# Kernel optimization log

Hardware: AMD Instinct MI355X
Metric: run time of the kernel (lower is better)

Reference implementation:

```python
import math
import jax, jax.numpy as jnp
import numpy as np

N_HEAD = 32
LAYER_NUMBER = 10  # cancels out: beta*alibi*L + alpha*QK^T*L = alibi + QK^T/sqrt(d)


def build_alibi(seq_len, n_head, dtype):
    # Faithful port of BLOOM's build_alibi_tensor -> [n_head, 1, seq_len]
    cp2 = 2 ** math.floor(math.log2(n_head))
    base = 2.0 ** (-(2.0 ** -(math.log2(cp2) - 3)))
    slopes = base ** np.arange(1, 1 + cp2)
    if cp2 != n_head:
        extra_base = 2.0 ** (-(2.0 ** -(math.log2(2 * cp2) - 3)))
        num_rem = min(cp2, n_head - cp2)
        slopes = np.concatenate([slopes, extra_base ** np.arange(1, 1 + 2 * num_rem, 2)])
    alibi = slopes[:, None, None] * np.arange(seq_len)[None, None, :]
    return jnp.asarray(alibi, dtype)


def setup_inputs() -> dict:
    key = jax.random.key(0)
    ks = jax.random.split(key, 6)
    B, S, H = 4, 1024, 4096
    return {
        "hidden_states": jax.random.normal(ks[0], (B, S, H), jnp.float32),
        "residual": jax.random.normal(ks[1], (B, S, H), jnp.float32),
        "qkv_w": jax.random.normal(ks[2], (3 * H, H), jnp.float32) * 0.02,
        "qkv_b": jnp.zeros((3 * H,), jnp.float32),
        "dense_w": jax.random.normal(ks[3], (H, H), jnp.float32) * 0.02,
        "dense_b": jnp.zeros((H,), jnp.float32),
    }


def reference(hidden_states, residual, qkv_w, qkv_b, dense_w, dense_b):
    B, S, H = hidden_states.shape
    nh = N_HEAD
    d = H // nh
    # fused qkv projection: [B,S,3H] -> [B,S,nh,3d] -> split
    mixed = (hidden_states @ qkv_w.T + qkv_b).reshape(B, S, nh, 3 * d)
    q, k, v = jnp.split(mixed, 3, axis=-1)  # each [B,S,nh,d]

    alibi = build_alibi(S, nh, hidden_states.dtype)  # [nh,1,S]
    # beta*alibi + alpha*QK^T, then *layer_number in scaled softmax == alibi + QK^T/sqrt(d)
    scores = jnp.einsum("bqhd,bkhd->bhqk", q, k) / math.sqrt(d) + alibi[None]  # [B,nh,S,S]

    causal = jnp.tril(jnp.ones((S, S), bool))  # [S,S], True = attend
    scores = jnp.where(causal, scores, jnp.asarray(-10000.0, scores.dtype))
    # softmax in fp32 (attention_softmax_in_fp32), then zero masked entries like *(~padded_causal_mask)
    probs = jax.nn.softmax(scores.astype(jnp.float32), axis=-1) * causal
    probs = probs.astype(v.dtype)

    ctx = jnp.einsum("bhqk,bkhd->bqhd", probs, v).reshape(B, S, H)
    out = ctx @ dense_w.T + dense_b + residual  # dropout_add with p=0 / eval
    return out
```

## Files before the change

kernel.cpp:

```cpp
#include <hip/hip_runtime.h>
#include <hip/hip_bf16.h>

typedef __attribute__((ext_vector_type(8))) short bf16x8;
typedef __attribute__((ext_vector_type(4))) short short4v;
typedef __attribute__((ext_vector_type(4))) float f32x4;

#define MFMA16(A, B, C) __builtin_amdgcn_mfma_f32_16x16x32_bf16((A), (B), (C), 0, 0, 0)
#define GLDS16(g, l)                                                            \
  __builtin_amdgcn_global_load_lds(                                             \
      (const __attribute__((address_space(1))) void*)(g),                       \
      (__attribute__((address_space(3))) void*)(l), 16, 0, 0)

__device__ __forceinline__ short f2bf(float f) {
  union { float f; unsigned u; } v; v.f = f;
  return (short)((v.u + 0x7fffu + ((v.u >> 16) & 1u)) >> 16);
}

__device__ __forceinline__ void blk_barrier() {
  asm volatile("" ::: "memory");
  __builtin_amdgcn_s_barrier();
  asm volatile("" ::: "memory");
}

__global__ __launch_bounds__(256) void cvt_kernel(const float* __restrict__ in,
                                                  short* __restrict__ out, int n4) {
  int i = blockIdx.x * 256 + threadIdx.x;
  const int stride = gridDim.x * 256;
  for (; i < n4; i += stride) {
    f32x4 v = ((const f32x4*)in)[i];
    short4v o;
    o[0] = f2bf(v[0]); o[1] = f2bf(v[1]); o[2] = f2bf(v[2]); o[3] = f2bf(v[3]);
    ((short4v*)out)[i] = o;
  }
}

__global__ __launch_bounds__(512, 2) void gemm_bt8(const short* __restrict__ A,
                                                   const short* __restrict__ B,
                                                   const float* __restrict__ bias,
                                                   const float* __restrict__ resid,
                                                   short* __restrict__ Cb,
                                                   float* __restrict__ Cf,
                                                   int Mtiles, int Nn, int K, int mode) {
  __shared__ short sA[2][2][8192];
  __shared__ short sB[2][2][8192];
  const int tid = threadIdx.x;
  const int w = tid >> 6, l = tid & 63;
  const int wm = w >> 2, wn = w & 3;
  const int fr = l & 15, g4 = l >> 4, sx = l & 7;

  const int nwg = gridDim.x;
  const int qq = nwg >> 3, rr = nwg & 7;
  const int xcd = blockIdx.x & 7, sub = blockIdx.x >> 3;
  const int swz = (xcd < rr ? xcd * (qq + 1) : rr * (qq + 1) + (xcd - rr) * qq) + sub;
  const int rowBase = (swz % Mtiles) * 256;
  const int colBase = (swz / Mtiles) * 256;

  const int NT = K >> 6;
  const int swcol = ((l & 7) ^ (l >> 3)) * 8;
  const short* Ag = A + (size_t)(rowBase + w * 8 + (l >> 3)) * K + swcol;
  const short* Bg = B + (size_t)(colBase + w * 8 + (l >> 3)) * K + swcol;
  const size_t q1 = (size_t)64 * K;
  const size_t hh = (size_t)128 * K;

#define STAGE_A(buf, h, ko)                                     \
  GLDS16(Ag + (h) * hh + (ko), &sA[buf][h][w * 512]);           \
  GLDS16(Ag + (h) * hh + q1 + (ko), &sA[buf][h][(8 + w) * 512]);
#define STAGE_B(buf, h, ko)                                     \
  GLDS16(Bg + (h) * hh + (ko), &sB[buf][h][w * 512]);           \
  GLDS16(Bg + (h) * hh + q1 + (ko), &sB[buf][h][(8 + w) * 512]);
#define RD_A(buf, m, ks) \
  (*(const bf16x8*)&sA[buf][wm][(((m) * 16 + fr) << 6) + ((((ks) * 4 + g4) ^ sx) << 3)])
#define RD_B(buf, nf, ks) \
  (*(const bf16x8*)&sB[buf][wn >> 1][((((wn & 1) * 64) + (nf) * 16 + fr) << 6) + ((((ks) * 4 + g4) ^ sx) << 3)])

  f32x4 acc[8][4];
#pragma unroll
  for (int m = 0; m < 8; m++)
#pragma unroll
    for (int n = 0; n < 4; n++) acc[m][n] = (f32x4)(0.0f);

  STAGE_A(0, 0, 0); STAGE_A(0, 1, 0);
  STAGE_B(0, 0, 0); STAGE_B(0, 1, 0);

  for (int t = 0; t < NT; ++t) {
    const int cur = t & 1, nxt = cur ^ 1;
    const size_t ko = (size_t)(t + 1) << 6;
    if (t + 1 < NT) {
      STAGE_A(nxt, 0, ko); STAGE_A(nxt, 1, ko);
      STAGE_B(nxt, 0, ko); STAGE_B(nxt, 1, ko);
      asm volatile("s_waitcnt vmcnt(8)" ::: "memory");
    } else {
      asm volatile("s_waitcnt vmcnt(0)" ::: "memory");
    }
    blk_barrier();

    bf16x8 bfr[4][2], af[2][2];
#pragma unroll
    for (int nf = 0; nf < 4; nf++) {
      bfr[nf][0] = RD_B(cur, nf, 0);
      bfr[nf][1] = RD_B(cur, nf, 1);
    }
    af[0][0] = RD_A(cur, 0, 0); af[0][1] = RD_A(cur, 0, 1);
    af[1][0] = RD_A(cur, 1, 0); af[1][1] = RD_A(cur, 1, 1);

#pragma unroll
    for (int p = 0; p < 4; p++) {
      bf16x8 afn[2][2];
      if (p < 3) {
        afn[0][0] = RD_A(cur, 2 * p + 2, 0); afn[0][1] = RD_A(cur, 2 * p + 2, 1);
        afn[1][0] = RD_A(cur, 2 * p + 3, 0); afn[1][1] = RD_A(cur, 2 * p + 3, 1);
      }
      __builtin_amdgcn_s_setprio(1);
#pragma unroll
      for (int ks2 = 0; ks2 < 2; ks2++)
#pragma unroll
        for (int mi = 0; mi < 2; mi++)
#pragma unroll
          for (int nf = 0; nf < 4; nf++)
            acc[2 * p + mi][nf] =
                MFMA16(af[mi][ks2], bfr[nf][ks2], acc[2 * p + mi][nf]);
      __builtin_amdgcn_s_setprio(0);
      if (p < 3) {
        af[0][0] = afn[0][0]; af[0][1] = afn[0][1];
        af[1][0] = afn[1][0]; af[1][1] = afn[1][1];
      }
      blk_barrier();
    }
  }

#pragma unroll
  for (int m = 0; m < 8; m++) {
    const int row0 = rowBase + wm * 128 + m * 16 + g4 * 4;
#pragma unroll
    for (int n = 0; n < 4; n++) {
      const int col = colBase + wn * 64 + n * 16 + fr;
      const float bc = bias[col];
#pragma unroll
      for (int j = 0; j < 4; j++) {
        const size_t idx = (size_t)(row0 + j) * Nn + col;
        const float v = acc[m][n][j] + bc;
        if (mode == 0) Cb[idx] = f2bf(v);
        else Cf[idx] = v + resid[idx];
      }
    }
  }
#undef STAGE_A
#undef STAGE_B
#undef RD_A
#undef RD_B
}

__global__ __launch_bounds__(256) void vtrans_kernel(const short* __restrict__ mixed,
                                                     short* __restrict__ vt) {
  __shared__ short tl[64][132];
  const int tid = threadIdx.x;
  const int st = blockIdx.x;
  const int bh = blockIdx.y;
  const int b = bh >> 5, h = bh & 31;
  const short* src = mixed + (size_t)(b * 1024 + st * 64) * 12288 + h * 384 + 256;
#pragma unroll
  for (int it = 0; it < 8; it++) {
    int idx = (tid + it * 256) * 4;
    int row = idx >> 7, col = idx & 127;
    *(short4v*)&tl[row][col] = *(const short4v*)(src + row * 12288 + col);
  }
  __syncthreads();
  short* dst = vt + (size_t)bh * 128 * 1024 + st * 64;
#pragma unroll
  for (int it = 0; it < 8; it++) {
    int o = (tid + it * 256) * 4;
    int d = o >> 6, t4 = o & 63;
    short4v w;
    w[0] = tl[t4][d]; w[1] = tl[t4 + 1][d]; w[2] = tl[t4 + 2][d]; w[3] = tl[t4 + 3][d];
    *(short4v*)(dst + d * 1024 + t4) = w;
  }
}

__global__ __launch_bounds__(256, 2) void attn_kernel(const short* __restrict__ mixed,
                                                      const short* __restrict__ vt,
                                                      short* __restrict__ ctx) {
  __shared__ short sK[2][64 * 128];
  __shared__ short sV[2][128 * 64];
  __shared__ unsigned p_lds[4][16 * 36];
  const int tid = threadIdx.x;
  const int w = tid >> 6, l = tid & 63;
  const int g = l >> 4, f = l & 15, f7 = l & 7;

  const int bidx = blockIdx.x;
  const int xcd = bidx & 7, idx = bidx >> 3;
  const int bh = (xcd << 4) | (idx >> 4);
  const int qt = idx & 15;
  const int b = bh >> 5, h = bh & 31;
  const int qw = qt * 64 + w * 16;
  const float scale = 0.08838834764831845f;
  const float slope = exp2f(-0.25f * (float)(h + 1));

  const short* qptr = mixed + (size_t)b * 1024 * 12288 + h * 384;
  const short* kptr = qptr + 128;
  const short* vtp = vt + (size_t)bh * 128 * 1024;

  bf16x8 qf[4];
  {
    const short* qrow = qptr + (size_t)(qw + f) * 12288 + (g << 3);
#pragma unroll
    for (int ks = 0; ks < 4; ks++) qf[ks] = *(const bf16x8*)(qrow + ks * 32);
  }

#define STAGE_K(buf, kt)                                                        \
  {                                                                             \
    _Pragma("unroll") for (int c4 = 0; c4 < 4; c4++) {                          \
      const int c = c4 * 4 + w;                                                 \
      const int r = c * 4 + (l >> 4);                                           \
      GLDS16(kptr + (size_t)((kt) + r) * 12288 + (((l & 15) ^ (r & 7)) << 3),   \
             &sK[buf][c << 9]);                                                 \
    }                                                                           \
  }
#define STAGE_V(buf, kt)                                                        \
  {                                                                             \
    _Pragma("unroll") for (int c4 = 0; c4 < 4; c4++) {                          \
      const int c = c4 * 4 + w;                                                 \
      const int r = c * 8 + (l >> 3);                                           \
      GLDS16(vtp + (size_t)r * 1024 + (kt) + (((l & 7) ^ (r & 7)) << 3),        \
             &sV[buf][c << 9]);                                                 \
    }                                                                           \
  }

  f32x4 acc[8];
#pragma unroll
  for (int n = 0; n < 8; n++) acc[n] = (f32x4)(0.0f);
  float mrun = -1e30f, lrun = 0.0f;
  const int q = qw + f;
  unsigned* pw = p_lds[w];

  const int TT = qt + 1;
  STAGE_K(0, 0);
  STAGE_V(0, 0);

  for (int t = 0; t < TT; ++t) {
    const int cur = t & 1, nxt = cur ^ 1;
    const int kt = t << 6;
    if (t + 1 < TT) {
      STAGE_K(nxt, kt + 64);
      STAGE_V(nxt, kt + 64);
      asm volatile("s_waitcnt vmcnt(8)" ::: "memory");
    } else {
      asm volatile("s_waitcnt vmcnt(0)" ::: "memory");
    }
    blk_barrier();

    f32x4 s[4];
#pragma unroll
    for (int ksub = 0; ksub < 4; ksub++) {
      s[ksub] = (f32x4)(0.0f);
      const int r = ksub * 16 + f;
#pragma unroll
      for (int ks = 0; ks < 4; ks++) {
        bf16x8 kf = *(const bf16x8*)&sK[cur][(r << 7) + ((((ks << 2) + g) ^ f7) << 3)];
        s[ksub] = MFMA16(kf, qf[ks], s[ksub]);
      }
    }

    float ev[4][4];
    float tmax = -1e30f;
#pragma unroll
    for (int ksub = 0; ksub < 4; ksub++)
#pragma unroll
      for (int j = 0; j < 4; j++) {
        const int k = kt + ksub * 16 + g * 4 + j;
        float v = s[ksub][j] * scale + slope * (float)k;
        if (k > q) v = -1e30f;
        ev[ksub][j] = v;
        tmax = fmaxf(tmax, v);
      }
    tmax = fmaxf(tmax, __shfl_xor(tmax, 16));
    tmax = fmaxf(tmax, __shfl_xor(tmax, 32));
    const float mnew = fmaxf(mrun, tmax);
    const float asc = __expf(mrun - mnew);
    float psum = 0.0f;
    unsigned* pr = pw + f * 36;
#pragma unroll
    for (int ksub = 0; ksub < 4; ksub++) {
      float e0 = __expf(ev[ksub][0] - mnew);
      float e1 = __expf(ev[ksub][1] - mnew);
      float e2 = __expf(ev[ksub][2] - mnew);
      float e3 = __expf(ev[ksub][3] - mnew);
      psum += (e0 + e1) + (e2 + e3);
      unsigned w0 = (unsigned)(unsigned short)f2bf(e0) |
                    ((unsigned)(unsigned short)f2bf(e1) << 16);
      unsigned w1 = (unsigned)(unsigned short)f2bf(e2) |
                    ((unsigned)(unsigned short)f2bf(e3) << 16);
      pr[ksub * 8 + g * 2] = w0;
      pr[ksub * 8 + g * 2 + 1] = w1;
    }
    psum += __shfl_xor(psum, 16);
    psum += __shfl_xor(psum, 32);
    lrun = lrun * asc + psum;
    mrun = mnew;

    float ascB[4];
#pragma unroll
    for (int j = 0; j < 4; j++) ascB[j] = __shfl(asc, 20 * g + j);
#pragma unroll
    for (int n = 0; n < 8; n++)
#pragma unroll
      for (int j = 0; j < 4; j++) acc[n][j] *= ascB[j];

    bf16x8 pa0 = *(const bf16x8*)(pw + f * 36 + (g << 2));
    bf16x8 pa1 = *(const bf16x8*)(pw + f * 36 + 16 + (g << 2));
#pragma unroll
    for (int n = 0; n < 8; n++) {
      const int dr = (n << 4) + f;
      bf16x8 vf0 = *(const bf16x8*)&sV[cur][(dr << 6) + ((g ^ f7) << 3)];
      acc[n] = MFMA16(pa0, vf0, acc[n]);
      bf16x8 vf1 = *(const bf16x8*)&sV[cur][(dr << 6) + (((4 + g) ^ f7) << 3)];
      acc[n] = MFMA16(pa1, vf1, acc[n]);
    }
    blk_barrier();
  }

  const float linv = 1.0f / lrun;
  float invB[4];
#pragma unroll
  for (int j = 0; j < 4; j++) invB[j] = __shfl(linv, 20 * g + j);
  const int trow = b * 1024 + qw + (g << 2);
#pragma unroll
  for (int n = 0; n < 8; n++) {
    const int col = h * 128 + (n << 4) + f;
#pragma unroll
    for (int j = 0; j < 4; j++)
      ctx[(size_t)(trow + j) * 4096 + col] = f2bf(acc[n][j] * invB[j]);
  }
#undef STAGE_K
#undef STAGE_V
}

extern "C" void kernel_launch(void* const* d_in, const int* in_sizes, int n_in,
                              void* d_out, int out_size, void* d_ws, size_t ws_size,
                              hipStream_t stream) {
  const float* hs = (const float*)d_in[0];
  const float* resid = (const float*)d_in[1];
  const float* qkv_w = (const float*)d_in[2];
  const float* qkv_b = (const float*)d_in[3];
  const float* dense_w = (const float*)d_in[4];
  const float* dense_b = (const float*)d_in[5];
  float* out = (float*)d_out;

  short* hs_b = (short*)d_ws;
  short* wqkv_b = hs_b + (size_t)16777216;
  short* wd_b = wqkv_b + (size_t)50331648;
  short* mixed = wd_b + (size_t)16777216;
  short* vt = wqkv_b;
  short* ctx = hs_b;

  cvt_kernel<<<1024, 256, 0, stream>>>(hs, hs_b, 16777216 / 4);
  cvt_kernel<<<1024, 256, 0, stream>>>(qkv_w, wqkv_b, 50331648 / 4);
  cvt_kernel<<<1024, 256, 0, stream>>>(dense_w, wd_b, 16777216 / 4);
  gemm_bt8<<<dim3(48 * 16), 512, 0, stream>>>(hs_b, wqkv_b, qkv_b, nullptr,
                                              mixed, nullptr, 16, 12288, 4096, 0);
  vtrans_kernel<<<dim3(16, 128), 256, 0, stream>>>(mixed, vt);
  attn_kernel<<<2048, 256, 0, stream>>>(mixed, vt, ctx);
  gemm_bt8<<<dim3(16 * 16), 512, 0, stream>>>(ctx, wd_b, dense_b, resid,
                                              nullptr, out, 16, 4096, 4096, 1);
}
```

Measured before the change: 918.4 us.

## Shrink GEMM tiles to 128x256 with K-step 32 and higher occupancy

Replaces the 256x256, K=64 GEMM with a 128x256 tile, K-step of 32, a smaller double-buffered LDS footprint, a new XOR swizzle and a 4-blocks-per-CU launch bound. Both projection GEMM launches double their grid size. The aim is more workgroups and better latency hiding through occupancy, instead of the deep intra-tile software pipelining with per-phase barriers. In exchange, each tile reuses operands less, there are twice as many barriers per K, and global and LDS traffic per FLOP rises.

```diff
diff --git a/kernel.cpp b/kernel.cpp
--- a/kernel.cpp
+++ b/kernel.cpp
@@ -34,103 +34,77 @@
   }
 }
 
-__global__ __launch_bounds__(512, 2) void gemm_bt8(const short* __restrict__ A,
-                                                   const short* __restrict__ B,
-                                                   const float* __restrict__ bias,
-                                                   const float* __restrict__ resid,
-                                                   short* __restrict__ Cb,
-                                                   float* __restrict__ Cf,
-                                                   int Mtiles, int Nn, int K, int mode) {
-  __shared__ short sA[2][2][8192];
-  __shared__ short sB[2][2][8192];
+__global__ __launch_bounds__(512, 4) void gemm_bt(const short* __restrict__ A,
+                                                  const short* __restrict__ B,
+                                                  const float* __restrict__ bias,
+                                                  const float* __restrict__ resid,
+                                                  short* __restrict__ Cb,
+                                                  float* __restrict__ Cf,
+                                                  int Mtiles, int Nn, int K, int mode) {
+  __shared__ short sA[2][128 * 32];
+  __shared__ short sB[2][256 * 32];
   const int tid = threadIdx.x;
   const int w = tid >> 6, l = tid & 63;
   const int wm = w >> 2, wn = w & 3;
-  const int fr = l & 15, g4 = l >> 4, sx = l & 7;
+  const int fr = l & 15, g4 = l >> 4;
+  const int slotx = (g4 ^ ((fr >> 1) & 3)) << 3;
 
   const int nwg = gridDim.x;
   const int qq = nwg >> 3, rr = nwg & 7;
   const int xcd = blockIdx.x & 7, sub = blockIdx.x >> 3;
   const int swz = (xcd < rr ? xcd * (qq + 1) : rr * (qq + 1) + (xcd - rr) * qq) + sub;
-  const int rowBase = (swz % Mtiles) * 256;
+  const int rowBase = (swz % Mtiles) * 128;
   const int colBase = (swz / Mtiles) * 256;
 
-  const int NT = K >> 6;
-  const int swcol = ((l & 7) ^ (l >> 3)) * 8;
-  const short* Ag = A + (size_t)(rowBase + w * 8 + (l >> 3)) * K + swcol;
-  const short* Bg = B + (size_t)(colBase + w * 8 + (l >> 3)) * K + swcol;
-  const size_t q1 = (size_t)64 * K;
-  const size_t hh = (size_t)128 * K;
-
-#define STAGE_A(buf, h, ko)                                     \
-  GLDS16(Ag + (h) * hh + (ko), &sA[buf][h][w * 512]);           \
-  GLDS16(Ag + (h) * hh + q1 + (ko), &sA[buf][h][(8 + w) * 512]);
-#define STAGE_B(buf, h, ko)                                     \
-  GLDS16(Bg + (h) * hh + (ko), &sB[buf][h][w * 512]);           \
-  GLDS16(Bg + (h) * hh + q1 + (ko), &sB[buf][h][(8 + w) * 512]);
-#define RD_A(buf, m, ks) \
-  (*(const bf16x8*)&sA[buf][wm][(((m) * 16 + fr) << 6) + ((((ks) * 4 + g4) ^ sx) << 3)])
-#define RD_B(buf, nf, ks) \
-  (*(const bf16x8*)&sB[buf][wn >> 1][((((wn & 1) * 64) + (nf) * 16 + fr) << 6) + ((((ks) * 4 + g4) ^ sx) << 3)])
-
-  f32x4 acc[8][4];
-#pragma unroll
-  for (int m = 0; m < 8; m++)
+  const int NT = K >> 5;
+  const int scol = ((l & 3) ^ ((l >> 3) & 3)) << 3;
+  const short* Ag = A + (size_t)(rowBase + w * 16 + (l >> 2)) * K + scol;
+  const short* Bg0 = B + (size_t)(colBase + w * 16 + (l >> 2)) * K + scol;
+  const short* Bg1 = Bg0 + (size_t)128 * K;
+
+  f32x4 acc[4][4];
+#pragma unroll
+  for (int m = 0; m < 4; m++)
 #pragma unroll
     for (int n = 0; n < 4; n++) acc[m][n] = (f32x4)(0.0f);
 
-  STAGE_A(0, 0, 0); STAGE_A(0, 1, 0);
-  STAGE_B(0, 0, 0); STAGE_B(0, 1, 0);
+  GLDS16(Ag, &sA[0][w * 512]);
+  GLDS16(Bg0, &sB[0][w * 512]);
+  GLDS16(Bg1, &sB[0][(8 + w) * 512]);
 
   for (int t = 0; t < NT; ++t) {
     const int cur = t & 1, nxt = cur ^ 1;
-    const size_t ko = (size_t)(t + 1) << 6;
+    const int ko = (t + 1) << 5;
     if (t + 1 < NT) {
-      STAGE_A(nxt, 0, ko); STAGE_A(nxt, 1, ko);
-      STAGE_B(nxt, 0, ko); STAGE_B(nxt, 1, ko);
-      asm volatile("s_waitcnt vmcnt(8)" ::: "memory");
+      GLDS16(Ag + ko, &sA[nxt][w * 512]);
+      GLDS16(Bg0 + ko, &sB[nxt][w * 512]);
+      GLDS16(Bg1 + ko, &sB[nxt][(8 + w) * 512]);
+      asm volatile("s_waitcnt vmcnt(3)" ::: "memory");
     } else {
       asm volatile("s_waitcnt vmcnt(0)" ::: "memory");
     }
     blk_barrier();
 
-    bf16x8 bfr[4][2], af[2][2];
-#pragma unroll
-    for (int nf = 0; nf < 4; nf++) {
-      bfr[nf][0] = RD_B(cur, nf, 0);
-      bfr[nf][1] = RD_B(cur, nf, 1);
-    }
-    af[0][0] = RD_A(cur, 0, 0); af[0][1] = RD_A(cur, 0, 1);
-    af[1][0] = RD_A(cur, 1, 0); af[1][1] = RD_A(cur, 1, 1);
-
-#pragma unroll
-    for (int p = 0; p < 4; p++) {
-      bf16x8 afn[2][2];
-      if (p < 3) {
-        afn[0][0] = RD_A(cur, 2 * p + 2, 0); afn[0][1] = RD_A(cur, 2 * p + 2, 1);
-        afn[1][0] = RD_A(cur, 2 * p + 3, 0); afn[1][1] = RD_A(cur, 2 * p + 3, 1);
-      }
-      __builtin_amdgcn_s_setprio(1);
-#pragma unroll
-      for (int ks2 = 0; ks2 < 2; ks2++)
-#pragma unroll
-        for (int mi = 0; mi < 2; mi++)
-#pragma unroll
-          for (int nf = 0; nf < 4; nf++)
-            acc[2 * p + mi][nf] =
-                MFMA16(af[mi][ks2], bfr[nf][ks2], acc[2 * p + mi][nf]);
-      __builtin_amdgcn_s_setprio(0);
-      if (p < 3) {
-        af[0][0] = afn[0][0]; af[0][1] = afn[0][1];
-        af[1][0] = afn[1][0]; af[1][1] = afn[1][1];
-      }
-      blk_barrier();
-    }
-  }
-
-#pragma unroll
-  for (int m = 0; m < 8; m++) {
-    const int row0 = rowBase + wm * 128 + m * 16 + g4 * 4;
+    bf16x8 af[4], bfr[4];
+#pragma unroll
+    for (int m = 0; m < 4; m++)
+      af[m] = *(const bf16x8*)&sA[cur][(wm * 64 + m * 16 + fr) * 32 + slotx];
+#pragma unroll
+    for (int nf = 0; nf < 4; nf++)
+      bfr[nf] = *(const bf16x8*)&sB[cur][(wn * 64 + nf * 16 + fr) * 32 + slotx];
+    __builtin_amdgcn_s_setprio(1);
+#pragma unroll
+    for (int m = 0; m < 4; m++)
+#pragma unroll
+      for (int nf = 0; nf < 4; nf++)
+        acc[m][nf] = MFMA16(af[m], bfr[nf], acc[m][nf]);
+    __builtin_amdgcn_s_setprio(0);
+    blk_barrier();
+  }
+
+#pragma unroll
+  for (int m = 0; m < 4; m++) {
+    const int row0 = rowBase + wm * 64 + m * 16 + g4 * 4;
 #pragma unroll
     for (int n = 0; n < 4; n++) {
       const int col = colBase + wn * 64 + n * 16 + fr;
@@ -144,10 +118,6 @@
       }
     }
   }
-#undef STAGE_A
-#undef STAGE_B
-#undef RD_A
-#undef RD_B
 }
 
 __global__ __launch_bounds__(256) void vtrans_kernel(const short* __restrict__ mixed,
@@ -355,10 +325,10 @@
   cvt_kernel<<<1024, 256, 0, stream>>>(hs, hs_b, 16777216 / 4);
   cvt_kernel<<<1024, 256, 0, stream>>>(qkv_w, wqkv_b, 50331648 / 4);
   cvt_kernel<<<1024, 256, 0, stream>>>(dense_w, wd_b, 16777216 / 4);
-  gemm_bt8<<<dim3(48 * 16), 512, 0, stream>>>(hs_b, wqkv_b, qkv_b, nullptr,
-                                              mixed, nullptr, 16, 12288, 4096, 0);
+  gemm_bt<<<dim3(32 * 48), 512, 0, stream>>>(hs_b, wqkv_b, qkv_b, nullptr,
+                                             mixed, nullptr, 32, 12288, 4096, 0);
   vtrans_kernel<<<dim3(16, 128), 256, 0, stream>>>(mixed, vt);
   attn_kernel<<<2048, 256, 0, stream>>>(mixed, vt, ctx);
-  gemm_bt8<<<dim3(16 * 16), 512, 0, stream>>>(ctx, wd_b, dense_b, resid,
-                                              nullptr, out, 16, 4096, 4096, 1);
-}
+  gemm_bt<<<dim3(32 * 16), 512, 0, stream>>>(ctx, wd_b, dense_b, resid,
+                                             nullptr, out, 32, 4096, 4096, 1);
+}
```

New measurement: 811.7 us. 11.6% less time.
